# Performance work log

Measured on AMD Instinct MI355X. Metric: run time of the kernel, lower is better.

The kernel has to match this reference:

```python
import jax, jax.numpy as jnp
import numpy as np

DIM = 512
NH, NKV, HD = 8, 4, DIM // 8
KVD = NKV * HD
EPS = 1.1920928955078125e-07  # torch.finfo(float32).eps (F.rms_norm default)
ROPE_BASE = 10000.0


def _rms_norm(x):
    # F.rms_norm over last dim, no learned weight
    ms = jnp.mean(jnp.square(x), axis=-1, keepdims=True)
    return x * jax.lax.rsqrt(ms + EPS)


def _rope_tables(T, dtype):
    inv_freq = 1.0 / (ROPE_BASE ** (jnp.arange(0, HD, 2, dtype=jnp.float32) / HD))
    t = jnp.arange(T, dtype=jnp.float32)
    f = jnp.outer(t, inv_freq)  # [T, HD//2]
    return jnp.cos(f).astype(dtype)[None, None], jnp.sin(f).astype(dtype)[None, None]


def _apply_rot(x, c, s):
    h = x.shape[-1] // 2
    x1, x2 = x[..., :h], x[..., h:]
    return jnp.concatenate((x1 * c + x2 * s, -x1 * s + x2 * c), axis=-1)


def setup_inputs() -> dict:
    key = jax.random.key(0)
    ks = jax.random.split(key, 5)
    B, T = 8, 2048
    x = jax.random.normal(ks[0], (B, T, DIM), dtype=jnp.float32)
    # torch Linear weights: [out_features, in_features]
    Wq = jax.random.normal(ks[1], (DIM, DIM), dtype=jnp.float32) * (DIM ** -0.5)
    Wk = jax.random.normal(ks[2], (KVD, DIM), dtype=jnp.float32) * (DIM ** -0.5)
    Wv = jax.random.normal(ks[3], (KVD, DIM), dtype=jnp.float32) * (DIM ** -0.5)
    Wp = jax.random.normal(ks[4], (DIM, DIM), dtype=jnp.float32) * (DIM ** -0.5)
    return {"x": x, "Wq": Wq, "Wk": Wk, "Wv": Wv, "Wp": Wp}


def reference(x, Wq, Wk, Wv, Wp):
    B, T, C = x.shape
    q = (x @ Wq.T).reshape(B, T, NH, HD).transpose(0, 2, 1, 3)    # [B,NH,T,HD]
    k = (x @ Wk.T).reshape(B, T, NKV, HD).transpose(0, 2, 1, 3)   # [B,NKV,T,HD]
    v = (x @ Wv.T).reshape(B, T, NKV, HD).transpose(0, 2, 1, 3)
    q, k = _rms_norm(q), _rms_norm(k)
    c, s = _rope_tables(T, q.dtype)
    q, k = _apply_rot(q, c, s), _apply_rot(k, c, s)
    rep = NH // NKV
    k = jnp.repeat(k, rep, axis=1)  # GQA expand -> [B,NH,T,HD]
    v = jnp.repeat(v, rep, axis=1)
    scale = 1.0 / jnp.sqrt(jnp.asarray(HD, dtype=q.dtype))
    scores = jnp.einsum('bhqd,bhkd->bhqk', q, k) * scale
    causal = jnp.tril(jnp.ones((T, T), dtype=bool))
    scores = jnp.where(causal[None, None], scores, jnp.finfo(scores.dtype).min)
    attn = jax.nn.softmax(scores, axis=-1)
    y = jnp.einsum('bhqk,bhkd->bhqd', attn, v)
    y = y.transpose(0, 2, 1, 3).reshape(B, T, C)
    return y @ Wp.T
```

## Files before the change

### kernel.cpp

```cpp
#include <hip/hip_runtime.h>
#include <hip/hip_bf16.h>
#include <stdint.h>

typedef __bf16 bf16;
typedef __bf16 bf16x8 __attribute__((ext_vector_type(8)));
typedef __bf16 bf16x4 __attribute__((ext_vector_type(4)));
typedef float f32x4 __attribute__((ext_vector_type(4)));

#define T_SEQ 2048
#define DIM_ 512
#define NH_ 8
#define NKV_ 4
#define HD_ 64
#define BT_ (8 * T_SEQ)
#define NEG_INF (-1e30f)
#define EPS_ 1.1920928955078125e-07f
#define QSCALE 0.18033688011112042f
#define SMAX 12.0f

#define OFF_XB   (size_t)(0)
#define OFF_WQKV (size_t)(16777216)
#define OFF_WP   (size_t)(17825792)
#define OFF_COS  (size_t)(18350080)
#define OFF_SIN  (size_t)(18612224)
#define OFF_QT   (size_t)(18874368)
#define OFF_KT   (size_t)(35651584)
#define OFF_VT   (size_t)(44040192)
#define OFF_Y    (size_t)(52428800)
#define WS_NEEDED (size_t)(69206016)

__device__ inline void mfma16(f32x4& acc, bf16x8 a, bf16x8 b) {
    acc = __builtin_amdgcn_mfma_f32_16x16x32_bf16(a, b, acc, 0, 0, 0);
}

typedef const __attribute__((address_space(1))) uint8_t* gas_ptr;
typedef __attribute__((address_space(3))) uint8_t* las_ptr;
__device__ inline void gload16(const bf16* g, bf16* l) {
    __builtin_amdgcn_global_load_lds((gas_ptr)(const void*)g, (las_ptr)(void*)l, 16, 0, 0);
}

__global__ void prep_kernel(const float* __restrict__ x, const float* __restrict__ wq,
                            const float* __restrict__ wk, const float* __restrict__ wv,
                            const float* __restrict__ wp,
                            bf16* __restrict__ xb, bf16* __restrict__ wqkv,
                            bf16* __restrict__ wpb, float* __restrict__ cosT,
                            float* __restrict__ sinT) {
    int tid = blockIdx.x * blockDim.x + threadIdx.x;
    int stride = gridDim.x * blockDim.x;
    for (int i = tid; i < BT_ * DIM_; i += stride) xb[i] = (bf16)x[i];
    for (int i = tid; i < 1024 * 512; i += stride) {
        int j = i >> 9, k = i & 511;
        float v;
        if (j < 512) v = wq[i];
        else if (j < 768) v = wk[(j - 512) * 512 + k];
        else v = wv[(j - 768) * 512 + k];
        wqkv[i] = (bf16)v;
    }
    for (int i = tid; i < 512 * 512; i += stride) wpb[i] = (bf16)wp[i];
    for (int i = tid; i < T_SEQ * 32; i += stride) {
        int t = i >> 5, d = i & 31;
        float inv = powf(10000.0f, -(float)d * (1.0f / 32.0f));
        float f = (float)t * inv;
        cosT[i] = cosf(f);
        sinT[i] = sinf(f);
    }
}

__global__ __launch_bounds__(256) void qkv_gemm(const bf16* __restrict__ A,
                                                const bf16* __restrict__ B,
                                                bf16* __restrict__ qt,
                                                bf16* __restrict__ kt,
                                                bf16* __restrict__ vt,
                                                const float* __restrict__ cosT,
                                                const float* __restrict__ sinT) {
    __shared__ __align__(16) char smem[34816];
    bf16* As = (bf16*)smem;
    bf16* Bs = (bf16*)(smem + 16384);
    const int tid = threadIdx.x, lane = tid & 63, wid = tid >> 6;
    const int wr = wid >> 1, wc = wid & 1;
    const int lm = lane & 15, hi = lane >> 4;
    const int bid = blockIdx.x;
    const int swz = (bid & 7) * 128 + (bid >> 3);
    const int brow = (swz & 127) * 128;
    const int bcol = (swz >> 7) * 128;

    f32x4 acc[4][4] = {};
    for (int k0 = 0; k0 < 512; k0 += 64) {
        __syncthreads();
#pragma unroll
        for (int i = 0; i < 4; ++i) {
            int c = i * 256 + tid;
            int slot = c >> 6, l = c & 63;
            int row = (slot >> 1) * 16 + (l & 15);
            int kc = (slot & 1) * 32 + (l >> 4) * 8;
            gload16(A + (size_t)(brow + row) * 512 + k0 + kc, As + c * 8);
            gload16(B + (size_t)(bcol + row) * 512 + k0 + kc, Bs + c * 8);
        }
        asm volatile("s_waitcnt vmcnt(0)" ::: "memory");
        __syncthreads();
#pragma unroll
        for (int kk = 0; kk < 2; ++kk) {
            bf16x8 af[4], bfr[4];
#pragma unroll
            for (int m = 0; m < 4; ++m)
                af[m] = *(const bf16x8*)(As + (((wr * 4 + m) * 2 + kk) * 64 + lane) * 8);
#pragma unroll
            for (int n = 0; n < 4; ++n)
                bfr[n] = *(const bf16x8*)(Bs + (((wc * 4 + n) * 2 + kk) * 64 + lane) * 8);
            __builtin_amdgcn_s_setprio(1);
#pragma unroll
            for (int m = 0; m < 4; ++m)
#pragma unroll
                for (int n = 0; n < 4; ++n) mfma16(acc[m][n], af[m], bfr[n]);
            __builtin_amdgcn_s_setprio(0);
        }
    }
    __syncthreads();

    bf16* Tb = (bf16*)smem + wid * 4224;
    const int wcol = bcol + wc * 64;
    const int ctype = (wcol < 512) ? 0 : (wcol < 768 ? 1 : 2);

    if (ctype < 2) {
#pragma unroll
        for (int m = 0; m < 4; ++m)
#pragma unroll
            for (int r = 0; r < 4; ++r) {
                float v0 = acc[m][0][r], v1 = acc[m][1][r];
                float v2 = acc[m][2][r], v3 = acc[m][3][r];
                float ss = v0 * v0 + v1 * v1 + v2 * v2 + v3 * v3;
                ss += __shfl_xor(ss, 1);
                ss += __shfl_xor(ss, 2);
                ss += __shfl_xor(ss, 4);
                ss += __shfl_xor(ss, 8);
                float rinv = rsqrtf(ss * (1.0f / 64.0f) + EPS_);
                v0 *= rinv; v1 *= rinv; v2 *= rinv; v3 *= rinv;
                int rl = m * 16 + hi * 4 + r;
                int t = (brow + wr * 64 + rl) & (T_SEQ - 1);
                float c0 = cosT[t * 32 + lm], s0 = sinT[t * 32 + lm];
                float c1 = cosT[t * 32 + 16 + lm], s1 = sinT[t * 32 + 16 + lm];
                float o0 = v0 * c0 + v2 * s0;
                float o2 = v2 * c0 - v0 * s0;
                float o1 = v1 * c1 + v3 * s1;
                float o3 = v3 * c1 - v1 * s1;
                if (ctype == 0) { o0 *= QSCALE; o1 *= QSCALE; o2 *= QSCALE; o3 *= QSCALE; }
                Tb[rl * 66 + lm]      = (bf16)o0;
                Tb[rl * 66 + 16 + lm] = (bf16)o1;
                Tb[rl * 66 + 32 + lm] = (bf16)o2;
                Tb[rl * 66 + 48 + lm] = (bf16)o3;
            }
    } else {
#pragma unroll
        for (int m = 0; m < 4; ++m)
#pragma unroll
            for (int n = 0; n < 4; ++n)
#pragma unroll
                for (int r = 0; r < 4; ++r)
                    Tb[(n * 16 + lm) * 66 + m * 16 + hi * 4 + r] = (bf16)acc[m][n][r];
    }
    __syncthreads();

    const int i0 = brow + wr * 64;
    const int b = i0 >> 11, tt = i0 & (T_SEQ - 1);
#pragma unroll
    for (int p = 0; p < 8; ++p) {
        int row = p * 8 + (lane >> 3);
        int ch = lane & 7;
        bf16x8 val = *(const bf16x8*)(Tb + row * 66 + ch * 8);
        if (ctype == 0) {
            int head = wcol >> 6;
            *(bf16x8*)(qt + ((size_t)((b << 3) + head) * T_SEQ + tt + row) * 64 + ch * 8) = val;
        } else if (ctype == 1) {
            int head = (wcol - 512) >> 6;
            *(bf16x8*)(kt + ((size_t)((b << 2) + head) * T_SEQ + tt + row) * 64 + ch * 8) = val;
        } else {
            int head = (wcol - 768) >> 6;
            *(bf16x8*)(vt + ((size_t)((b << 2) + head) * 64 + row) * T_SEQ + tt + ch * 8) = val;
        }
    }
}

__global__ __launch_bounds__(256, 4) void attn_kernel(const bf16* __restrict__ qt,
                                                      const bf16* __restrict__ kt,
                                                      const bf16* __restrict__ vt,
                                                      bf16* __restrict__ y) {
    __shared__ bf16 Klds[4096];
    __shared__ bf16 Vlds[4096];
    __shared__ bf16 Plds[4][1152];
    const int tid = threadIdx.x;
    const int lane = tid & 63, wid = tid >> 6;
    const int lm = lane & 15, hi = lane >> 4;
    const int bid = blockIdx.x;
    const int s8 = bid >> 8;
    const int g4 = (bid >> 6) & 3;
    const int bh = bid & 63;
    const int p = 4 * (7 - s8) + ((g4 + s8) & 3);
    const int b = bh >> 3, h = bh & 7, hv = h >> 1;
    const bf16* Q = qt + (size_t)bh * T_SEQ * HD_;
    const bf16* K = kt + (size_t)(b * NKV_ + hv) * T_SEQ * HD_;
    const bf16* V = vt + (size_t)(b * NKV_ + hv) * HD_ * T_SEQ;
    const int qB = p * 64;
    const int qw = qB + wid * 16;
    bf16* Pl = &Plds[wid][0];

    const int sl0 = tid >> 6, l0 = tid & 63;
    const int gr0 = (sl0 >> 1) * 16 + (l0 & 15);
    const int gc0 = (sl0 & 1) * 32 + (l0 >> 4) * 8;
    const int sl1 = (256 + tid) >> 6;
    const int gr1 = (sl1 >> 1) * 16 + (l0 & 15);
    const int gc1 = (sl1 & 1) * 32 + (l0 >> 4) * 8;
    const bf16* kg0 = K + (size_t)gr0 * HD_ + gc0;
    const bf16* kg1 = K + (size_t)gr1 * HD_ + gc1;
    const bf16* vg0 = V + (size_t)gr0 * T_SEQ + gc0;
    const bf16* vg1 = V + (size_t)gr1 * T_SEQ + gc1;
    bf16* kd0 = Klds + (size_t)tid * 8;
    bf16* kd1 = Klds + (size_t)(256 + tid) * 8;
    bf16* vd0 = Vlds + (size_t)tid * 8;
    bf16* vd1 = Vlds + (size_t)(256 + tid) * 8;

    bf16x8 qf[2];
#pragma unroll
    for (int kk = 0; kk < 2; ++kk)
        qf[kk] = *(const bf16x8*)(Q + (size_t)(qw + lm) * HD_ + 32 * kk + 8 * hi);

    bf16x8 vones;
#pragma unroll
    for (int j = 0; j < 8; ++j) vones[j] = (bf16)1.0f;

    f32x4 o[4] = {};
    f32x4 lacc = {};

    const int nt = p + 1;
    for (int t = 0; t < nt; ++t) {
        const int kv0 = t << 6;
        __syncthreads();
        {
            size_t ko = (size_t)kv0 * HD_, vo = (size_t)kv0;
            gload16(kg0 + ko, kd0);
            gload16(kg1 + ko, kd1);
            gload16(vg0 + vo, vd0);
            gload16(vg1 + vo, vd1);
        }
        asm volatile("s_waitcnt vmcnt(0)" ::: "memory");
        __syncthreads();

        if (kv0 <= qw + 15) {
            f32x4 s[4] = {};
#pragma unroll
            for (int kk = 0; kk < 2; ++kk) {
                bf16x8 kf[4];
#pragma unroll
                for (int n = 0; n < 4; ++n)
                    kf[n] = *(const bf16x8*)(Klds + ((n * 2 + kk) * 64 + lane) * 8);
#pragma unroll
                for (int n = 0; n < 4; ++n) mfma16(s[n], kf[n], qf[kk]);
            }
            const bool partial = (kv0 + 63 > qw);
            const int qg = qw + lm;
            bf16x4 pw[4];
#pragma unroll
            for (int n = 0; n < 4; ++n)
#pragma unroll
                for (int r = 0; r < 4; ++r) {
                    float xv = s[n][r];
                    if (partial)
                        xv = ((kv0 + 16 * n + 4 * hi + r) <= qg) ? xv : NEG_INF;
                    pw[n][r] = (bf16)__builtin_amdgcn_exp2f(xv - SMAX);
                }
#pragma unroll
            for (int kk = 0; kk < 2; ++kk) {
                *(bf16x4*)(Pl + lm * 40 + 4 * hi)      = pw[2 * kk];
                *(bf16x4*)(Pl + lm * 40 + 16 + 4 * hi) = pw[2 * kk + 1];
                bf16x8 vf[4], pf;
                pf = *(const bf16x8*)(Pl + lm * 40 + 8 * hi);
#pragma unroll
                for (int nd = 0; nd < 4; ++nd)
                    vf[nd] = *(const bf16x8*)(Vlds + ((nd * 2 + kk) * 64 + lane) * 8);
#pragma unroll
                for (int nd = 0; nd < 4; ++nd) mfma16(o[nd], vf[nd], pf);
                mfma16(lacc, vones, pf);
            }
        }
    }

    float rcl = 1.0f / lacc[0];
#pragma unroll
    for (int nd = 0; nd < 4; ++nd) {
        bf16x4 ov;
#pragma unroll
        for (int r = 0; r < 4; ++r) ov[r] = (bf16)(o[nd][r] * rcl);
        *(bf16x4*)(Pl + lm * 72 + nd * 16 + 4 * hi) = ov;
    }
#pragma unroll
    for (int it = 0; it < 2; ++it) {
        int chunk = it * 64 + lane;
        int row = chunk >> 3, dc = (chunk & 7) * 8;
        bf16x8 val = *(const bf16x8*)(Pl + row * 72 + dc);
        *(bf16x8*)(y + (size_t)(b * T_SEQ + qw + row) * DIM_ + h * HD_ + dc) = val;
    }
}

__global__ __launch_bounds__(256) void proj_gemm(const bf16* __restrict__ A,
                                                 const bf16* __restrict__ B,
                                                 float* __restrict__ out) {
    __shared__ __align__(16) char smem[32768];
    bf16* As = (bf16*)smem;
    bf16* Bs = (bf16*)(smem + 16384);
    const int tid = threadIdx.x, lane = tid & 63, wid = tid >> 6;
    const int wr = wid >> 1, wc = wid & 1;
    const int lm = lane & 15, hi = lane >> 4;
    const int bid = blockIdx.x;
    const int swz = (bid & 7) * 64 + (bid >> 3);
    const int brow = (swz & 127) * 128;
    const int bcol = (swz >> 7) * 128;

    f32x4 acc[4][4] = {};
    for (int k0 = 0; k0 < 512; k0 += 64) {
        __syncthreads();
#pragma unroll
        for (int i = 0; i < 4; ++i) {
            int c = i * 256 + tid;
            int slot = c >> 6, l = c & 63;
            int row = (slot >> 1) * 16 + (l & 15);
            int kc = (slot & 1) * 32 + (l >> 4) * 8;
            gload16(A + (size_t)(brow + row) * 512 + k0 + kc, As + c * 8);
            gload16(B + (size_t)(bcol + row) * 512 + k0 + kc, Bs + c * 8);
        }
        asm volatile("s_waitcnt vmcnt(0)" ::: "memory");
        __syncthreads();
#pragma unroll
        for (int kk = 0; kk < 2; ++kk) {
            bf16x8 af[4], bfr[4];
#pragma unroll
            for (int m = 0; m < 4; ++m)
                af[m] = *(const bf16x8*)(As + (((wr * 4 + m) * 2 + kk) * 64 + lane) * 8);
#pragma unroll
            for (int n = 0; n < 4; ++n)
                bfr[n] = *(const bf16x8*)(Bs + (((wc * 4 + n) * 2 + kk) * 64 + lane) * 8);
            __builtin_amdgcn_s_setprio(1);
#pragma unroll
            for (int m = 0; m < 4; ++m)
#pragma unroll
                for (int n = 0; n < 4; ++n) mfma16(acc[m][n], af[m], bfr[n]);
            __builtin_amdgcn_s_setprio(0);
        }
    }
#pragma unroll
    for (int m = 0; m < 4; ++m)
#pragma unroll
        for (int n = 0; n < 4; ++n)
#pragma unroll
            for (int r = 0; r < 4; ++r) {
                int i = brow + wr * 64 + m * 16 + hi * 4 + r;
                int j = bcol + wc * 64 + n * 16 + lm;
                out[(size_t)i * DIM_ + j] = acc[m][n][r];
            }
}

extern "C" void kernel_launch(void* const* d_in, const int* in_sizes, int n_in,
                              void* d_out, int out_size, void* d_ws, size_t ws_size,
                              hipStream_t stream) {
    const float* x  = (const float*)d_in[0];
    const float* wq = (const float*)d_in[1];
    const float* wk = (const float*)d_in[2];
    const float* wv = (const float*)d_in[3];
    const float* wp = (const float*)d_in[4];
    if (ws_size < WS_NEEDED) return;

    char* ws = (char*)d_ws;
    bf16* xb    = (bf16*)(ws + OFF_XB);
    bf16* wqkv  = (bf16*)(ws + OFF_WQKV);
    bf16* wpb   = (bf16*)(ws + OFF_WP);
    float* cosT = (float*)(ws + OFF_COS);
    float* sinT = (float*)(ws + OFF_SIN);
    bf16* qt    = (bf16*)(ws + OFF_QT);
    bf16* kt    = (bf16*)(ws + OFF_KT);
    bf16* vt    = (bf16*)(ws + OFF_VT);
    bf16* y     = (bf16*)(ws + OFF_Y);

    prep_kernel<<<2048, 256, 0, stream>>>(x, wq, wk, wv, wp, xb, wqkv, wpb, cosT, sinT);

    qkv_gemm<<<1024, 256, 0, stream>>>(xb, wqkv, qt, kt, vt, cosT, sinT);

    attn_kernel<<<2048, 256, 0, stream>>>(qt, kt, vt, y);

    proj_gemm<<<512, 256, 0, stream>>>(y, wpb, (float*)d_out);
}
```

Measured before the change: 147.7 us.

## Fuse fp32-to-bf16 conversion into GEMM loads and retile projection GEMM

Removes the separate prep pass that converted x and the weights to bf16. The QKV and projection GEMMs now read fp32 directly, convert in registers and store bf16 into LDS, so the prep kernel only builds the RoPE tables. The projection GEMM switches to 128x64 tiles with twice as many blocks. This saves a full read and write of x, but replaces async global-to-LDS loads with synchronous register loads. It also reads x at twice the bytes once for each column tile, since each x row tile is loaded by 8 column blocks.

```diff
diff --git a/kernel.cpp b/kernel.cpp
--- a/kernel.cpp
+++ b/kernel.cpp
@@ -18,9 +18,6 @@
 #define QSCALE 0.18033688011112042f
 #define SMAX 12.0f
 
-#define OFF_XB   (size_t)(0)
-#define OFF_WQKV (size_t)(16777216)
-#define OFF_WP   (size_t)(17825792)
 #define OFF_COS  (size_t)(18350080)
 #define OFF_SIN  (size_t)(18612224)
 #define OFF_QT   (size_t)(18874368)
@@ -39,24 +36,16 @@
     __builtin_amdgcn_global_load_lds((gas_ptr)(const void*)g, (las_ptr)(void*)l, 16, 0, 0);
 }
 
-__global__ void prep_kernel(const float* __restrict__ x, const float* __restrict__ wq,
-                            const float* __restrict__ wk, const float* __restrict__ wv,
-                            const float* __restrict__ wp,
-                            bf16* __restrict__ xb, bf16* __restrict__ wqkv,
-                            bf16* __restrict__ wpb, float* __restrict__ cosT,
-                            float* __restrict__ sinT) {
+__device__ inline bf16x8 cvt8(const float4& a, const float4& b) {
+    bf16x8 v;
+    v[0] = (bf16)a.x; v[1] = (bf16)a.y; v[2] = (bf16)a.z; v[3] = (bf16)a.w;
+    v[4] = (bf16)b.x; v[5] = (bf16)b.y; v[6] = (bf16)b.z; v[7] = (bf16)b.w;
+    return v;
+}
+
+__global__ void prep_kernel(float* __restrict__ cosT, float* __restrict__ sinT) {
     int tid = blockIdx.x * blockDim.x + threadIdx.x;
     int stride = gridDim.x * blockDim.x;
-    for (int i = tid; i < BT_ * DIM_; i += stride) xb[i] = (bf16)x[i];
-    for (int i = tid; i < 1024 * 512; i += stride) {
-        int j = i >> 9, k = i & 511;
-        float v;
-        if (j < 512) v = wq[i];
-        else if (j < 768) v = wk[(j - 512) * 512 + k];
-        else v = wv[(j - 768) * 512 + k];
-        wqkv[i] = (bf16)v;
-    }
-    for (int i = tid; i < 512 * 512; i += stride) wpb[i] = (bf16)wp[i];
     for (int i = tid; i < T_SEQ * 32; i += stride) {
         int t = i >> 5, d = i & 31;
         float inv = powf(10000.0f, -(float)d * (1.0f / 32.0f));
@@ -66,8 +55,10 @@
     }
 }
 
-__global__ __launch_bounds__(256) void qkv_gemm(const bf16* __restrict__ A,
-                                                const bf16* __restrict__ B,
+__global__ __launch_bounds__(256) void qkv_gemm(const float* __restrict__ X,
+                                                const float* __restrict__ wq,
+                                                const float* __restrict__ wk,
+                                                const float* __restrict__ wv,
                                                 bf16* __restrict__ qt,
                                                 bf16* __restrict__ kt,
                                                 bf16* __restrict__ vt,
@@ -83,6 +74,10 @@
     const int swz = (bid & 7) * 128 + (bid >> 3);
     const int brow = (swz & 127) * 128;
     const int bcol = (swz >> 7) * 128;
+    const float* Wsrc; int bofs;
+    if (bcol < 512) { Wsrc = wq; bofs = bcol; }
+    else if (bcol < 768) { Wsrc = wk; bofs = bcol - 512; }
+    else { Wsrc = wv; bofs = bcol - 768; }
 
     f32x4 acc[4][4] = {};
     for (int k0 = 0; k0 < 512; k0 += 64) {
@@ -93,10 +88,13 @@
             int slot = c >> 6, l = c & 63;
             int row = (slot >> 1) * 16 + (l & 15);
             int kc = (slot & 1) * 32 + (l >> 4) * 8;
-            gload16(A + (size_t)(brow + row) * 512 + k0 + kc, As + c * 8);
-            gload16(B + (size_t)(bcol + row) * 512 + k0 + kc, Bs + c * 8);
-        }
-        asm volatile("s_waitcnt vmcnt(0)" ::: "memory");
+            const float* ap = X + (size_t)(brow + row) * 512 + k0 + kc;
+            const float* bp = Wsrc + (size_t)(bofs + row) * 512 + k0 + kc;
+            float4 a0 = *(const float4*)ap, a1 = *(const float4*)(ap + 4);
+            float4 b0 = *(const float4*)bp, b1 = *(const float4*)(bp + 4);
+            *(bf16x8*)(As + c * 8) = cvt8(a0, a1);
+            *(bf16x8*)(Bs + c * 8) = cvt8(b0, b1);
+        }
         __syncthreads();
 #pragma unroll
         for (int kk = 0; kk < 2; ++kk) {
@@ -301,20 +299,20 @@
 }
 
 __global__ __launch_bounds__(256) void proj_gemm(const bf16* __restrict__ A,
-                                                 const bf16* __restrict__ B,
+                                                 const float* __restrict__ Wp,
                                                  float* __restrict__ out) {
-    __shared__ __align__(16) char smem[32768];
+    __shared__ __align__(16) char smem[24576];
     bf16* As = (bf16*)smem;
     bf16* Bs = (bf16*)(smem + 16384);
     const int tid = threadIdx.x, lane = tid & 63, wid = tid >> 6;
     const int wr = wid >> 1, wc = wid & 1;
     const int lm = lane & 15, hi = lane >> 4;
     const int bid = blockIdx.x;
-    const int swz = (bid & 7) * 64 + (bid >> 3);
+    const int swz = (bid & 7) * 128 + (bid >> 3);
     const int brow = (swz & 127) * 128;
-    const int bcol = (swz >> 7) * 128;
-
-    f32x4 acc[4][4] = {};
+    const int bcol = (swz >> 7) * 64;
+
+    f32x4 acc[4][2] = {};
     for (int k0 = 0; k0 < 512; k0 += 64) {
         __syncthreads();
 #pragma unroll
@@ -324,35 +322,44 @@
             int row = (slot >> 1) * 16 + (l & 15);
             int kc = (slot & 1) * 32 + (l >> 4) * 8;
             gload16(A + (size_t)(brow + row) * 512 + k0 + kc, As + c * 8);
-            gload16(B + (size_t)(bcol + row) * 512 + k0 + kc, Bs + c * 8);
+        }
+#pragma unroll
+        for (int i = 0; i < 2; ++i) {
+            int c = i * 256 + tid;
+            int slot = c >> 6, l = c & 63;
+            int row = (slot >> 1) * 16 + (l & 15);
+            int kc = (slot & 1) * 32 + (l >> 4) * 8;
+            const float* bp = Wp + (size_t)(bcol + row) * 512 + k0 + kc;
+            float4 b0 = *(const float4*)bp, b1 = *(const float4*)(bp + 4);
+            *(bf16x8*)(Bs + c * 8) = cvt8(b0, b1);
         }
         asm volatile("s_waitcnt vmcnt(0)" ::: "memory");
         __syncthreads();
 #pragma unroll
         for (int kk = 0; kk < 2; ++kk) {
-            bf16x8 af[4], bfr[4];
+            bf16x8 af[4], bfr[2];
 #pragma unroll
             for (int m = 0; m < 4; ++m)
                 af[m] = *(const bf16x8*)(As + (((wr * 4 + m) * 2 + kk) * 64 + lane) * 8);
 #pragma unroll
-            for (int n = 0; n < 4; ++n)
-                bfr[n] = *(const bf16x8*)(Bs + (((wc * 4 + n) * 2 + kk) * 64 + lane) * 8);
+            for (int n = 0; n < 2; ++n)
+                bfr[n] = *(const bf16x8*)(Bs + (((wc * 2 + n) * 2 + kk) * 64 + lane) * 8);
             __builtin_amdgcn_s_setprio(1);
 #pragma unroll
             for (int m = 0; m < 4; ++m)
 #pragma unroll
-                for (int n = 0; n < 4; ++n) mfma16(acc[m][n], af[m], bfr[n]);
+                for (int n = 0; n < 2; ++n) mfma16(acc[m][n], af[m], bfr[n]);
             __builtin_amdgcn_s_setprio(0);
         }
     }
 #pragma unroll
     for (int m = 0; m < 4; ++m)
 #pragma unroll
-        for (int n = 0; n < 4; ++n)
+        for (int n = 0; n < 2; ++n)
 #pragma unroll
             for (int r = 0; r < 4; ++r) {
                 int i = brow + wr * 64 + m * 16 + hi * 4 + r;
-                int j = bcol + wc * 64 + n * 16 + lm;
+                int j = bcol + wc * 32 + n * 16 + lm;
                 out[(size_t)i * DIM_ + j] = acc[m][n][r];
             }
 }
@@ -368,9 +375,6 @@
     if (ws_size < WS_NEEDED) return;
 
     char* ws = (char*)d_ws;
-    bf16* xb    = (bf16*)(ws + OFF_XB);
-    bf16* wqkv  = (bf16*)(ws + OFF_WQKV);
-    bf16* wpb   = (bf16*)(ws + OFF_WP);
     float* cosT = (float*)(ws + OFF_COS);
     float* sinT = (float*)(ws + OFF_SIN);
     bf16* qt    = (bf16*)(ws + OFF_QT);
@@ -378,11 +382,11 @@
     bf16* vt    = (bf16*)(ws + OFF_VT);
     bf16* y     = (bf16*)(ws + OFF_Y);
 
-    prep_kernel<<<2048, 256, 0, stream>>>(x, wq, wk, wv, wp, xb, wqkv, wpb, cosT, sinT);
-
-    qkv_gemm<<<1024, 256, 0, stream>>>(xb, wqkv, qt, kt, vt, cosT, sinT);
+    prep_kernel<<<64, 256, 0, stream>>>(cosT, sinT);
+
+    qkv_gemm<<<1024, 256, 0, stream>>>(x, wq, wk, wv, qt, kt, vt, cosT, sinT);
 
     attn_kernel<<<2048, 256, 0, stream>>>(qt, kt, vt, y);
 
-    proj_gemm<<<512, 256, 0, stream>>>(y, wpb, (float*)d_out);
-}
+    proj_gemm<<<1024, 256, 0, stream>>>(y, wp, (float*)d_out);
+}
```

Result: slower. 187.6 us (+27.0%).
